# Kernel tuning notes

Measured on AMD Instinct MI355X. Metric: run time of the kernel, lower is better.

## Reference

```python
import jax, jax.numpy as jnp
import numpy as np

N_NODES = 200000
N_EDGES = 6400000
IN_CH = 256
HID = 16


def gcn_conv(h, src, dst, deg_inv_sqrt, W, b, n_nodes):
    """One GCNConv (PyG semantics: add self-loops, symmetric norm, linear, scatter-add, bias)."""
    hw = h @ W  # [N, out]
    norm = deg_inv_sqrt[src] * deg_inv_sqrt[dst]  # [E]
    agg = jax.ops.segment_sum(norm[:, None] * hw[src], dst, num_segments=n_nodes)
    # self-loop contribution: deg_inv_sqrt[i]^2 * hw[i]
    agg = agg + hw * (deg_inv_sqrt ** 2)[:, None]
    return agg + b


def setup_inputs() -> dict:
    key = jax.random.key(0)
    k_x, k_e, k_w1, k_w2, k_w3 = jax.random.split(key, 5)
    x = jax.random.normal(k_x, (N_NODES, IN_CH), dtype=jnp.float32)
    edge_index = jax.random.randint(k_e, (2, N_EDGES), 0, N_NODES, dtype=jnp.int64)
    # Glorot-ish init for the three GCNConv weights, zeros for biases (PyG default)
    W1 = jax.random.normal(k_w1, (IN_CH, HID), dtype=jnp.float32) * (1.0 / np.sqrt(IN_CH))
    b1 = jnp.zeros((HID,), dtype=jnp.float32)
    W2 = jax.random.normal(k_w2, (HID, HID), dtype=jnp.float32) * (1.0 / np.sqrt(HID))
    b2 = jnp.zeros((HID,), dtype=jnp.float32)
    W3 = jax.random.normal(k_w3, (HID, 1), dtype=jnp.float32) * (1.0 / np.sqrt(HID))
    b3 = jnp.zeros((1,), dtype=jnp.float32)
    return {"x": x, "edge_index": edge_index, "W1": W1, "b1": b1,
            "W2": W2, "b2": b2, "W3": W3, "b3": b3}


def reference(x, edge_index, W1, b1, W2, b2, W3, b3):
    n_nodes = x.shape[0]
    src, dst = edge_index[0], edge_index[1]
    # GCN norm with self-loops: deg counts incoming edges + 1 self-loop
    deg = jax.ops.segment_sum(jnp.ones_like(dst, dtype=x.dtype), dst,
                              num_segments=n_nodes) + 1.0
    deg_inv_sqrt = deg ** -0.5  # deg >= 1, safe
    h = jax.nn.relu(gcn_conv(x, src, dst, deg_inv_sqrt, W1, b1, n_nodes))
    # dropout is identity in eval mode
    h = jax.nn.relu(gcn_conv(h, src, dst, deg_inv_sqrt, W2, b2, n_nodes))
    out = gcn_conv(h, src, dst, deg_inv_sqrt, W3, b3, n_nodes)  # [N, 1]
    return out
```

## Files before the change

kernel.cpp:

```cpp
#include <hip/hip_runtime.h>

#define NN 200000
#define EE 6400000L
#define NCB 196
#define CAP 36864
#define TILE 8192
#define NTILE 782

__device__ inline void f4add(float4& a, const float4 v) {
    a.x += v.x; a.y += v.y; a.z += v.z; a.w += v.w;
}

__global__ void k_detect(const int* __restrict__ w, int* __restrict__ flag,
                         int* __restrict__ gcur) {
    __shared__ int any;
    if (threadIdx.x == 0) any = 0;
    __syncthreads();
    int found = 0;
    for (int i = threadIdx.x; i < 8192; i += 256)
        if (w[2 * i + 1] != 0) found = 1;
    if (found) atomicOr(&any, 1);
    if (threadIdx.x < NCB) gcur[threadIdx.x] = threadIdx.x * CAP;
    __syncthreads();
    if (threadIdx.x == 0) flag[0] = any ? 0 : 1;
}

__global__ __launch_bounds__(256) void k_passA(
    const int* __restrict__ ew, const int* __restrict__ flag,
    int* __restrict__ gcur, unsigned* __restrict__ stage, long e) {
    __shared__ unsigned lv[TILE];
    __shared__ unsigned char lb[TILE];
    __shared__ int lh[NCB], lseg[NCB], lcur[NCB];
    for (int i = threadIdx.x; i < NCB; i += 256) { lh[i] = 0; lcur[i] = 0; }
    __syncthreads();
    long t0 = (long)blockIdx.x * TILE;
    int cnt = (int)min((long)TILE, e - t0);
    int shift = *flag;
    for (int i = threadIdx.x; i < cnt; i += 256) {
        int s = ew[(t0 + i) << shift];
        int d = ew[(EE + t0 + i) << shift];
        int b = d >> 10;
        lv[i] = (unsigned)s | ((unsigned)(d & 1023) << 18);
        lb[i] = (unsigned char)b;
        atomicAdd(&lh[b], 1);
    }
    __syncthreads();
    for (int i = threadIdx.x; i < NCB; i += 256)
        if (lh[i]) lseg[i] = atomicAdd(&gcur[i], lh[i]);
    __syncthreads();
    for (int i = threadIdx.x; i < cnt; i += 256) {
        int b = lb[i];
        int r = atomicAdd(&lcur[b], 1);
        stage[lseg[b] + r] = lv[i];
    }
}

__global__ __launch_bounds__(1024) void k_sortB(
    const unsigned* __restrict__ stage, const int* __restrict__ gcur,
    float* __restrict__ dis, int2* __restrict__ odn,
    unsigned* __restrict__ csr, int n) {
    __shared__ int cnt[1024];
    __shared__ int cur[1024];
    __shared__ int wsum[16];
    int t = threadIdx.x, B = blockIdx.x;
    cnt[t] = 0;
    __syncthreads();
    int s0 = B * CAP, s1 = gcur[B];
    for (int i = s0 + t; i < s1; i += 1024)
        atomicAdd(&cnt[stage[i] >> 18], 1);
    __syncthreads();
    int c = cnt[t];
    int pc = (c + 3) & ~3;
    int lane = t & 63, w = t >> 6;
    int s = pc;
#pragma unroll
    for (int o = 1; o < 64; o <<= 1) {
        int u = __shfl_up(s, o, 64);
        if (lane >= o) s += u;
    }
    if (lane == 63) wsum[w] = s;
    __syncthreads();
    int add = 0;
    for (int k = 0; k < w; ++k) add += wsum[k];
    int excl = s - pc + add;
    cur[t] = excl;
    int node = B * 1024 + t;
    if (node < n) {
        odn[node] = make_int2(s0 + excl, c);
        dis[node] = rsqrtf((float)(c + 1));
    }
    __syncthreads();
    for (int i = s0 + t; i < s1; i += 1024) {
        unsigned v = stage[i];
        int pos = s0 + atomicAdd(&cur[v >> 18], 1);
        csr[pos] = v & 0x3FFFF;
    }
}

__global__ __launch_bounds__(256) void k_mm1(
    const float* __restrict__ x, const float* __restrict__ W,
    const float* __restrict__ dis, float4* __restrict__ outr, int n) {
    __shared__ float Wl[256 * 16];
    int t = threadIdx.x;
#pragma unroll
    for (int i = 0; i < 4; ++i)
        ((float4*)Wl)[t + i * 256] = ((const float4*)W)[t + i * 256];
    __syncthreads();

    int node = blockIdx.x * 256 + t;
    if (node >= n) return;

    const float4* xr = (const float4*)(x + (long)node * 256);
    float acc[16];
#pragma unroll
    for (int o = 0; o < 16; ++o) acc[o] = 0.f;

#pragma unroll 8
    for (int kk = 0; kk < 64; ++kk) {
        float4 xv = xr[kk];
#pragma unroll
        for (int q = 0; q < 4; ++q) {
            float xs = (q == 0) ? xv.x : (q == 1) ? xv.y : (q == 2) ? xv.z : xv.w;
            const float4* wr = (const float4*)&Wl[(kk * 4 + q) * 16];
#pragma unroll
            for (int oo = 0; oo < 4; ++oo) {
                float4 wv = wr[oo];
                acc[oo * 4 + 0] = fmaf(xs, wv.x, acc[oo * 4 + 0]);
                acc[oo * 4 + 1] = fmaf(xs, wv.y, acc[oo * 4 + 1]);
                acc[oo * 4 + 2] = fmaf(xs, wv.z, acc[oo * 4 + 2]);
                acc[oo * 4 + 3] = fmaf(xs, wv.w, acc[oo * 4 + 3]);
            }
        }
    }
    float dv = dis[node];
#pragma unroll
    for (int q = 0; q < 4; ++q)
        outr[node * 4 + q] = make_float4(acc[q * 4] * dv, acc[q * 4 + 1] * dv,
                                         acc[q * 4 + 2] * dv, acc[q * 4 + 3] * dv);
}

__global__ __launch_bounds__(256) void k_g16a(
    const int2* __restrict__ odn, const unsigned* __restrict__ csr,
    const float* __restrict__ dis, const float4* __restrict__ tab,
    const float* __restrict__ b1v, const float* __restrict__ W2,
    float4* __restrict__ out2) {
    __shared__ float h1s[64 * 17];
    __shared__ float W2l[256];
    int t = threadIdx.x;
    if (t < 64) ((float4*)W2l)[t] = ((const float4*)W2)[t];
    int node = blockIdx.x * 64 + (t >> 2);
    int j = t & 3;
    int2 od = odn[node];
    int s0 = od.x, dg = od.y;
    float4 aA = make_float4(0.f, 0.f, 0.f, 0.f);
    float4 aB = make_float4(0.f, 0.f, 0.f, 0.f);
    int k = 0;
    for (; k + 8 <= dg; k += 8) {
        uint4 eL = *(const uint4*)(csr + s0 + k);
        uint4 eH = *(const uint4*)(csr + s0 + k + 4);
        f4add(aA, tab[eL.x * 4 + j]);
        f4add(aB, tab[eH.x * 4 + j]);
        f4add(aA, tab[eL.y * 4 + j]);
        f4add(aB, tab[eH.y * 4 + j]);
        f4add(aA, tab[eL.z * 4 + j]);
        f4add(aB, tab[eH.z * 4 + j]);
        f4add(aA, tab[eL.w * 4 + j]);
        f4add(aB, tab[eH.w * 4 + j]);
    }
    if (k + 4 <= dg) {
        uint4 e = *(const uint4*)(csr + s0 + k);
        f4add(aA, tab[e.x * 4 + j]);
        f4add(aB, tab[e.y * 4 + j]);
        f4add(aA, tab[e.z * 4 + j]);
        f4add(aB, tab[e.w * 4 + j]);
        k += 4;
    }
    for (; k < dg; ++k)
        f4add(aA, tab[csr[s0 + k] * 4 + j]);
    f4add(aA, aB);
    f4add(aA, tab[node * 4 + j]);
    float dv = dis[node];
    float4 bb = ((const float4*)b1v)[j];
    float4 r = make_float4(fmaf(dv, aA.x, bb.x), fmaf(dv, aA.y, bb.y),
                           fmaf(dv, aA.z, bb.z), fmaf(dv, aA.w, bb.w));
    r.x = fmaxf(r.x, 0.f); r.y = fmaxf(r.y, 0.f);
    r.z = fmaxf(r.z, 0.f); r.w = fmaxf(r.w, 0.f);
    int nl = t >> 2;
    h1s[nl * 17 + 4 * j + 0] = r.x;
    h1s[nl * 17 + 4 * j + 1] = r.y;
    h1s[nl * 17 + 4 * j + 2] = r.z;
    h1s[nl * 17 + 4 * j + 3] = r.w;
    __syncthreads();
    float4 acc = make_float4(0.f, 0.f, 0.f, 0.f);
#pragma unroll
    for (int kk = 0; kk < 16; ++kk) {
        float hv = h1s[nl * 17 + kk];
        float4 wv = ((const float4*)&W2l[kk * 16])[j];
        acc.x = fmaf(hv, wv.x, acc.x);
        acc.y = fmaf(hv, wv.y, acc.y);
        acc.z = fmaf(hv, wv.z, acc.z);
        acc.w = fmaf(hv, wv.w, acc.w);
    }
    out2[(long)node * 4 + j] = make_float4(acc.x * dv, acc.y * dv,
                                           acc.z * dv, acc.w * dv);
}

__global__ __launch_bounds__(256) void k_g16b(
    const int2* __restrict__ odn, const unsigned* __restrict__ csr,
    const float* __restrict__ dis, const float4* __restrict__ tab,
    const float* __restrict__ b2v, const float* __restrict__ W3,
    float* __restrict__ hws3) {
    int t = threadIdx.x;
    int node = blockIdx.x * 64 + (t >> 2);
    int j = t & 3;
    int2 od = odn[node];
    int s0 = od.x, dg = od.y;
    float4 aA = make_float4(0.f, 0.f, 0.f, 0.f);
    float4 aB = make_float4(0.f, 0.f, 0.f, 0.f);
    int k = 0;
    for (; k + 8 <= dg; k += 8) {
        uint4 eL = *(const uint4*)(csr + s0 + k);
        uint4 eH = *(const uint4*)(csr + s0 + k + 4);
        f4add(aA, tab[eL.x * 4 + j]);
        f4add(aB, tab[eH.x * 4 + j]);
        f4add(aA, tab[eL.y * 4 + j]);
        f4add(aB, tab[eH.y * 4 + j]);
        f4add(aA, tab[eL.z * 4 + j]);
        f4add(aB, tab[eH.z * 4 + j]);
        f4add(aA, tab[eL.w * 4 + j]);
        f4add(aB, tab[eH.w * 4 + j]);
    }
    if (k + 4 <= dg) {
        uint4 e = *(const uint4*)(csr + s0 + k);
        f4add(aA, tab[e.x * 4 + j]);
        f4add(aB, tab[e.y * 4 + j]);
        f4add(aA, tab[e.z * 4 + j]);
        f4add(aB, tab[e.w * 4 + j]);
        k += 4;
    }
    for (; k < dg; ++k)
        f4add(aA, tab[csr[s0 + k] * 4 + j]);
    f4add(aA, aB);
    f4add(aA, tab[node * 4 + j]);
    float dv = dis[node];
    float4 bb = ((const float4*)b2v)[j];
    float4 r = make_float4(fmaf(dv, aA.x, bb.x), fmaf(dv, aA.y, bb.y),
                           fmaf(dv, aA.z, bb.z), fmaf(dv, aA.w, bb.w));
    r.x = fmaxf(r.x, 0.f); r.y = fmaxf(r.y, 0.f);
    r.z = fmaxf(r.z, 0.f); r.w = fmaxf(r.w, 0.f);
    float4 w3 = ((const float4*)W3)[j];
    float pd = r.x * w3.x + r.y * w3.y + r.z * w3.z + r.w * w3.w;
    pd += __shfl_xor(pd, 1, 4);
    pd += __shfl_xor(pd, 2, 4);
    if (j == 0) hws3[node] = pd * dv;
}

__global__ __launch_bounds__(256) void k_g1(
    const int2* __restrict__ odn, const unsigned* __restrict__ csr,
    const float* __restrict__ dis, const float* __restrict__ hws3,
    const float* __restrict__ b, float* __restrict__ out, int n) {
    int t = threadIdx.x;
    int node = blockIdx.x * 16 + (t >> 4);
    int ln = t & 15;
    if (node >= n) return;
    int2 od = odn[node];
    int s0 = od.x, dg = od.y;
    float acc = 0.f;
    for (int k = ln; k < dg; k += 16)
        acc += hws3[csr[s0 + k]];
#pragma unroll
    for (int o = 8; o >= 1; o >>= 1) acc += __shfl_down(acc, o, 16);
    if (ln == 0)
        out[node] = fmaf(dis[node], acc + hws3[node], b[0]);
}

extern "C" void kernel_launch(void* const* d_in, const int* in_sizes, int n_in,
                              void* d_out, int out_size, void* d_ws, size_t ws_size,
                              hipStream_t stream) {
    const float* x  = (const float*)d_in[0];
    const int*   ew = (const int*)d_in[1];
    const float* W1 = (const float*)d_in[2];
    const float* b1 = (const float*)d_in[3];
    const float* W2 = (const float*)d_in[4];
    const float* b2 = (const float*)d_in[5];
    const float* W3 = (const float*)d_in[6];
    const float* b3 = (const float*)d_in[7];
    float* out = (float*)d_out;

    unsigned* stage = (unsigned*)d_ws;
    unsigned* csr   = stage + (long)NCB * CAP;
    int*      gcur  = (int*)(csr + (long)NCB * CAP);
    int*      flag  = gcur + 256;
    int2*     odn   = (int2*)(flag + 16);
    float*    dis   = (float*)(odn + 200704);
    float4*   bufA  = (float4*)(dis + 200704);
    float4*   bufB  = bufA + 4 * 200064;

    const int n = NN;
    const long e = EE;
    int nb = (n + 255) / 256;
    int gb = n / 64;
    int g1b = n / 16;

    k_detect<<<1, 256, 0, stream>>>(ew, flag, gcur);
    k_passA<<<NTILE, 256, 0, stream>>>(ew, flag, gcur, stage, e);
    k_sortB<<<NCB, 1024, 0, stream>>>(stage, gcur, dis, odn, csr, n);
    k_mm1<<<nb, 256, 0, stream>>>(x, W1, dis, bufA, n);
    k_g16a<<<gb, 256, 0, stream>>>(odn, csr, dis, bufA, b1, W2, bufB);
    k_g16b<<<gb, 256, 0, stream>>>(odn, csr, dis, bufB, b2, W3, (float*)bufA);
    k_g1<<<g1b, 256, 0, stream>>>(odn, csr, dis, (const float*)bufA, b3, out, n);
}
```

Before: 433.8 us.

## Reorder gather nodes by degree via histogram permutation for load balance

Builds a degree histogram in the sort kernel, scans it, and uses a counting sort to produce a node permutation grouped by in-degree. The three gather kernels then process nodes in that order, so threads in a wavefront have similar loop trip counts and less divergence. It adds two small kernels and an indirection load per node, and makes output writes scattered rather than contiguous.

```diff
diff --git a/kernel.cpp b/kernel.cpp
--- a/kernel.cpp
+++ b/kernel.cpp
@@ -12,7 +12,7 @@
 }
 
 __global__ void k_detect(const int* __restrict__ w, int* __restrict__ flag,
-                         int* __restrict__ gcur) {
+                         int* __restrict__ gcur, int* __restrict__ dhist) {
     __shared__ int any;
     if (threadIdx.x == 0) any = 0;
     __syncthreads();
@@ -21,6 +21,7 @@
         if (w[2 * i + 1] != 0) found = 1;
     if (found) atomicOr(&any, 1);
     if (threadIdx.x < NCB) gcur[threadIdx.x] = threadIdx.x * CAP;
+    for (int i = threadIdx.x; i < 1024; i += 256) dhist[i] = 0;
     __syncthreads();
     if (threadIdx.x == 0) flag[0] = any ? 0 : 1;
 }
@@ -58,12 +59,14 @@
 __global__ __launch_bounds__(1024) void k_sortB(
     const unsigned* __restrict__ stage, const int* __restrict__ gcur,
     float* __restrict__ dis, int2* __restrict__ odn,
-    unsigned* __restrict__ csr, int n) {
+    unsigned* __restrict__ csr, int* __restrict__ dhist, int n) {
     __shared__ int cnt[1024];
     __shared__ int cur[1024];
+    __shared__ int lhist[1024];
     __shared__ int wsum[16];
     int t = threadIdx.x, B = blockIdx.x;
     cnt[t] = 0;
+    lhist[t] = 0;
     __syncthreads();
     int s0 = B * CAP, s1 = gcur[B];
     for (int i = s0 + t; i < s1; i += 1024)
@@ -88,13 +91,46 @@
     if (node < n) {
         odn[node] = make_int2(s0 + excl, c);
         dis[node] = rsqrtf((float)(c + 1));
-    }
-    __syncthreads();
+        atomicAdd(&lhist[min(c, 1023)], 1);
+    }
+    __syncthreads();
+    if (lhist[t]) atomicAdd(&dhist[t], lhist[t]);
     for (int i = s0 + t; i < s1; i += 1024) {
         unsigned v = stage[i];
         int pos = s0 + atomicAdd(&cur[v >> 18], 1);
         csr[pos] = v & 0x3FFFF;
     }
+}
+
+__global__ __launch_bounds__(1024) void k_dscan(
+    const int* __restrict__ dhist, int* __restrict__ dbase, int* __restrict__ dcur) {
+    __shared__ int wsum[16];
+    int t = threadIdx.x;
+    int v = dhist[t];
+    int lane = t & 63, w = t >> 6;
+    int s = v;
+#pragma unroll
+    for (int o = 1; o < 64; o <<= 1) {
+        int u = __shfl_up(s, o, 64);
+        if (lane >= o) s += u;
+    }
+    if (lane == 63) wsum[w] = s;
+    __syncthreads();
+    int add = 0;
+    for (int k = 0; k < w; ++k) add += wsum[k];
+    int excl = s - v + add;
+    dbase[t] = excl;
+    dcur[t] = excl;
+}
+
+__global__ __launch_bounds__(256) void k_perm(
+    const int2* __restrict__ odn, int* __restrict__ dcur,
+    int* __restrict__ perm, int n) {
+    int i = blockIdx.x * 256 + threadIdx.x;
+    if (i >= n) return;
+    int c = min(odn[i].y, 1023);
+    int pos = atomicAdd(&dcur[c], 1);
+    perm[pos] = i;
 }
 
 __global__ __launch_bounds__(256) void k_mm1(
@@ -140,15 +176,15 @@
 }
 
 __global__ __launch_bounds__(256) void k_g16a(
-    const int2* __restrict__ odn, const unsigned* __restrict__ csr,
-    const float* __restrict__ dis, const float4* __restrict__ tab,
-    const float* __restrict__ b1v, const float* __restrict__ W2,
-    float4* __restrict__ out2) {
+    const int* __restrict__ perm, const int2* __restrict__ odn,
+    const unsigned* __restrict__ csr, const float* __restrict__ dis,
+    const float4* __restrict__ tab, const float* __restrict__ b1v,
+    const float* __restrict__ W2, float4* __restrict__ out2) {
     __shared__ float h1s[64 * 17];
     __shared__ float W2l[256];
     int t = threadIdx.x;
     if (t < 64) ((float4*)W2l)[t] = ((const float4*)W2)[t];
-    int node = blockIdx.x * 64 + (t >> 2);
+    int node = perm[blockIdx.x * 64 + (t >> 2)];
     int j = t & 3;
     int2 od = odn[node];
     int s0 = od.x, dg = od.y;
@@ -206,12 +242,12 @@
 }
 
 __global__ __launch_bounds__(256) void k_g16b(
-    const int2* __restrict__ odn, const unsigned* __restrict__ csr,
-    const float* __restrict__ dis, const float4* __restrict__ tab,
-    const float* __restrict__ b2v, const float* __restrict__ W3,
-    float* __restrict__ hws3) {
-    int t = threadIdx.x;
-    int node = blockIdx.x * 64 + (t >> 2);
+    const int* __restrict__ perm, const int2* __restrict__ odn,
+    const unsigned* __restrict__ csr, const float* __restrict__ dis,
+    const float4* __restrict__ tab, const float* __restrict__ b2v,
+    const float* __restrict__ W3, float* __restrict__ hws3) {
+    int t = threadIdx.x;
+    int node = perm[blockIdx.x * 64 + (t >> 2)];
     int j = t & 3;
     int2 od = odn[node];
     int s0 = od.x, dg = od.y;
@@ -256,13 +292,13 @@
 }
 
 __global__ __launch_bounds__(256) void k_g1(
-    const int2* __restrict__ odn, const unsigned* __restrict__ csr,
-    const float* __restrict__ dis, const float* __restrict__ hws3,
-    const float* __restrict__ b, float* __restrict__ out, int n) {
-    int t = threadIdx.x;
-    int node = blockIdx.x * 16 + (t >> 4);
+    const int* __restrict__ perm, const int2* __restrict__ odn,
+    const unsigned* __restrict__ csr, const float* __restrict__ dis,
+    const float* __restrict__ hws3, const float* __restrict__ b,
+    float* __restrict__ out) {
+    int t = threadIdx.x;
+    int node = perm[blockIdx.x * 16 + (t >> 4)];
     int ln = t & 15;
-    if (node >= n) return;
     int2 od = odn[node];
     int s0 = od.x, dg = od.y;
     float acc = 0.f;
@@ -291,7 +327,11 @@
     unsigned* csr   = stage + (long)NCB * CAP;
     int*      gcur  = (int*)(csr + (long)NCB * CAP);
     int*      flag  = gcur + 256;
-    int2*     odn   = (int2*)(flag + 16);
+    int*      dhist = flag + 16;
+    int*      dbase = dhist + 1024;
+    int*      dcur  = dbase + 1024;
+    int*      perm  = dcur + 1024;
+    int2*     odn   = (int2*)(perm + 200704);
     float*    dis   = (float*)(odn + 200704);
     float4*   bufA  = (float4*)(dis + 200704);
     float4*   bufB  = bufA + 4 * 200064;
@@ -302,11 +342,13 @@
     int gb = n / 64;
     int g1b = n / 16;
 
-    k_detect<<<1, 256, 0, stream>>>(ew, flag, gcur);
+    k_detect<<<1, 256, 0, stream>>>(ew, flag, gcur, dhist);
     k_passA<<<NTILE, 256, 0, stream>>>(ew, flag, gcur, stage, e);
-    k_sortB<<<NCB, 1024, 0, stream>>>(stage, gcur, dis, odn, csr, n);
+    k_sortB<<<NCB, 1024, 0, stream>>>(stage, gcur, dis, odn, csr, dhist, n);
+    k_dscan<<<1, 1024, 0, stream>>>(dhist, dbase, dcur);
+    k_perm<<<nb, 256, 0, stream>>>(odn, dcur, perm, n);
     k_mm1<<<nb, 256, 0, stream>>>(x, W1, dis, bufA, n);
-    k_g16a<<<gb, 256, 0, stream>>>(odn, csr, dis, bufA, b1, W2, bufB);
-    k_g16b<<<gb, 256, 0, stream>>>(odn, csr, dis, bufB, b2, W3, (float*)bufA);
-    k_g1<<<g1b, 256, 0, stream>>>(odn, csr, dis, (const float*)bufA, b3, out, n);
-}
+    k_g16a<<<gb, 256, 0, stream>>>(perm, odn, csr, dis, bufA, b1, W2, bufB);
+    k_g16b<<<gb, 256, 0, stream>>>(perm, odn, csr, dis, bufB, b2, W3, (float*)bufA);
+    k_g1<<<g1b, 256, 0, stream>>>(perm, odn, csr, dis, (const float*)bufA, b3, out);
+}
```

New measurement: 919.2 us. +111.9%, slower.
